# Kernel optimization log

Hardware: AMD Instinct MI355X
Metric: run time of the kernel (lower is better)

Reference implementation:

```python
import jax, jax.numpy as jnp
import numpy as np

B, T, D = 8, 2048, 1024
E, S = 8, 1            # num_experts, num_slots
FF = 4 * (S * D)       # ffn_mult * (num_slots * hiddens)

def setup_inputs() -> dict:
    key = jax.random.key(0)
    ks = jax.random.split(key, 7)
    sd = S * D
    inp = {
        "X":  jax.random.normal(ks[0], (B, T, D), dtype=jnp.float32),
        # slots gating MLP (single linear D -> E*S)
        "Wg": jax.random.normal(ks[1], (D, E * S), dtype=jnp.float32) / np.sqrt(D),
        "bg": jnp.zeros((E * S,), dtype=jnp.float32),
        # expert FFN (weights SHARED across experts, as in source [FFN(...)]*E)
        "W1": jax.random.normal(ks[2], (sd, FF), dtype=jnp.float32) / np.sqrt(sd),
        "b1": jnp.zeros((FF,), dtype=jnp.float32),
        "W2": jax.random.normal(ks[3], (FF, sd), dtype=jnp.float32) / np.sqrt(FF),
        "b2": jnp.zeros((sd,), dtype=jnp.float32),
    }
    return inp

def reference(X, Wg, bg, W1, b1, W2, b2):
    # logits: (B, T, E*S)
    logits = jnp.einsum('btd,de->bte', X, Wg) + bg
    dispatch_w = jax.nn.softmax(logits, axis=1)   # over tokens T
    combine_w = jax.nn.softmax(logits, axis=2)    # over slots E*S
    # slots = dispatch_w^T @ X : (B, E*S, D) -> (B, E, S*D)
    slots = jnp.einsum('bte,btd->bed', dispatch_w, X).reshape(B, E, S * D)
    # shared-weight FFN applied per expert slot (dropout=0 at eval)
    h = jax.nn.silu(jnp.einsum('bef,fh->beh', slots, W1) + b1)
    y = jnp.einsum('beh,hf->bef', h, W2) + b2     # (B, E, S*D)
    y = y.reshape(B, E * S, D)
    # combine: (B, T, E*S) @ (B, E*S, D)
    return jnp.einsum('bte,bed->btd', combine_w, y)
```

## Files before the change

kernel.cpp:

```cpp
#include <hip/hip_runtime.h>
#include <math.h>

#define B_  8
#define T_  2048
#define D_  1024
#define E_  8
#define FF_ 4096
#define N_  64
#define BT_ (B_*T_)

__global__ __launch_bounds__(256) void k_logits_part(
    const float* __restrict__ X, const float* __restrict__ Wg,
    float* __restrict__ part)
{
    __shared__ float xt[256 * 36];

    const int tid = threadIdx.x;
    const int bt0 = blockIdx.x * 256;
    const int d0  = blockIdx.y * 128;

    float acc[8];
    #pragma unroll
    for (int e = 0; e < 8; ++e) acc[e] = 0.f;

    for (int dt = 0; dt < 4; ++dt) {
        if (dt) __syncthreads();
        #pragma unroll
        for (int r = 0; r < 8; ++r) {
            int fi = r * 256 + tid;
            int token = fi >> 3, dj = fi & 7;
            const float4 v = *(const float4*)
                &X[(size_t)(bt0 + token) * D_ + d0 + dt * 32 + dj * 4];
            *(float4*)&xt[token * 36 + dj * 4] = v;
        }
        __syncthreads();
        #pragma unroll
        for (int dj = 0; dj < 8; ++dj) {
            const float4 x4 = *(const float4*)&xt[tid * 36 + dj * 4];
            const int db = d0 + dt * 32 + dj * 4;
            const float xv[4] = {x4.x, x4.y, x4.z, x4.w};
            #pragma unroll
            for (int r = 0; r < 4; ++r) {
                const float4 wlo = *(const float4*)&Wg[(size_t)(db + r) * 8];
                const float4 whi = *(const float4*)&Wg[(size_t)(db + r) * 8 + 4];
                acc[0] += xv[r] * wlo.x; acc[1] += xv[r] * wlo.y;
                acc[2] += xv[r] * wlo.z; acc[3] += xv[r] * wlo.w;
                acc[4] += xv[r] * whi.x; acc[5] += xv[r] * whi.y;
                acc[6] += xv[r] * whi.z; acc[7] += xv[r] * whi.w;
            }
        }
    }

    float* pp = &part[(size_t)blockIdx.y * BT_ * E_ + (size_t)(bt0 + tid) * E_];
    *(float4*)&pp[0] = make_float4(acc[0], acc[1], acc[2], acc[3]);
    *(float4*)&pp[4] = make_float4(acc[4], acc[5], acc[6], acc[7]);
}

__global__ __launch_bounds__(256) void k_logits_merge(
    const float* __restrict__ part, const float* __restrict__ bg,
    float* __restrict__ logits, float* __restrict__ sexp_part)
{
    __shared__ float red[8 * 256];
    const int tid = threadIdx.x;
    const int token = blockIdx.x * 256 + tid;

    float a[8];
    #pragma unroll
    for (int e = 0; e < 8; ++e) a[e] = 0.f;
    #pragma unroll
    for (int p = 0; p < 8; ++p) {
        const float* pp = &part[(size_t)p * BT_ * E_ + (size_t)token * E_];
        const float4 v0 = *(const float4*)&pp[0];
        const float4 v1 = *(const float4*)&pp[4];
        a[0] += v0.x; a[1] += v0.y; a[2] += v0.z; a[3] += v0.w;
        a[4] += v1.x; a[5] += v1.y; a[6] += v1.z; a[7] += v1.w;
    }
    #pragma unroll
    for (int e = 0; e < 8; ++e) a[e] += bg[e];

    float* lp = &logits[(size_t)token * E_];
    *(float4*)&lp[0] = make_float4(a[0], a[1], a[2], a[3]);
    *(float4*)&lp[4] = make_float4(a[4], a[5], a[6], a[7]);

    #pragma unroll
    for (int e = 0; e < 8; ++e) red[e * 256 + tid] = expf(a[e]);
    __syncthreads();
    for (int s = 128; s >= 1; s >>= 1) {
        if (tid < s) {
            #pragma unroll
            for (int e = 0; e < 8; ++e)
                red[e * 256 + tid] += red[e * 256 + tid + s];
        }
        __syncthreads();
    }
    if (tid < 8) sexp_part[blockIdx.x * 8 + tid] = red[tid * 256];
}

__global__ __launch_bounds__(256) void k_slots_part(
    const float* __restrict__ X, const float* __restrict__ logits,
    const float* __restrict__ sexp_part, float* __restrict__ part)
{
    __shared__ float wlds[64 * 8];
    __shared__ float red[64];
    __shared__ float inv[8];

    const int tid = threadIdx.x;
    const int ts = blockIdx.x, b = blockIdx.y;
    const int t0 = ts * 64;

    if (tid < 64) red[tid] = sexp_part[b * 64 + tid];
    __syncthreads();
    if (tid < 8) {
        float s = 0.f;
        #pragma unroll
        for (int i = 0; i < 8; ++i) s += red[i * 8 + tid];
        inv[tid] = 1.f / s;
    }
    __syncthreads();
    #pragma unroll
    for (int r = 0; r < 2; ++r) {
        int idx = r * 256 + tid;
        wlds[idx] = expf(logits[((size_t)b * T_ + t0) * E_ + idx]) * inv[idx & 7];
    }
    __syncthreads();

    float4 acc[8];
    #pragma unroll
    for (int e = 0; e < 8; ++e) { acc[e].x = acc[e].y = acc[e].z = acc[e].w = 0.f; }

    const float* xb = &X[((size_t)b * T_ + t0) * D_ + tid * 4];
    #pragma unroll 8
    for (int t = 0; t < 64; ++t) {
        const float4 x4 = *(const float4*)&xb[(size_t)t * D_];
        const float4 wA = *(const float4*)&wlds[t * 8];
        const float4 wB = *(const float4*)&wlds[t * 8 + 4];
        const float w[8] = {wA.x, wA.y, wA.z, wA.w, wB.x, wB.y, wB.z, wB.w};
        #pragma unroll
        for (int e = 0; e < 8; ++e) {
            acc[e].x += x4.x * w[e];
            acc[e].y += x4.y * w[e];
            acc[e].z += x4.z * w[e];
            acc[e].w += x4.w * w[e];
        }
    }
    #pragma unroll
    for (int e = 0; e < 8; ++e) {
        *(float4*)&part[(size_t)ts * (N_ * D_) + (size_t)(b * E_ + e) * D_ + tid * 4] = acc[e];
    }
}

__global__ __launch_bounds__(256) void k_reduce_slots(
    const float* __restrict__ part, float* __restrict__ slots)
{
    const int i = blockIdx.x * 256 + threadIdx.x;
    float s = 0.f;
    #pragma unroll
    for (int p = 0; p < 32; ++p) s += part[(size_t)p * (N_ * D_) + i];
    slots[i] = s;
}

__global__ __launch_bounds__(256) void k_gemm_part(
    const float* __restrict__ A, const float* __restrict__ W,
    float* __restrict__ part, int K, int F)
{
    __shared__ float As[64][128];

    const int tid = threadIdx.x;
    const int rg  = tid >> 5;
    const int cg  = tid & 31;
    const int f0  = blockIdx.x * 128 + cg * 4;
    const int k0  = blockIdx.y * 128;

    #pragma unroll
    for (int i = 0; i < 8; ++i) {
        int idx = i * 256 + tid;
        int row = idx >> 5, kq = idx & 31;
        const float4 v = *(const float4*)&A[(size_t)row * K + k0 + kq * 4];
        *(float4*)&As[row][kq * 4] = v;
    }
    __syncthreads();

    float4 acc[8];
    #pragma unroll
    for (int r = 0; r < 8; ++r) { acc[r].x = acc[r].y = acc[r].z = acc[r].w = 0.f; }

    #pragma unroll 2
    for (int kq = 0; kq < 32; ++kq) {
        float4 w0 = *(const float4*)&W[(size_t)(k0 + kq * 4 + 0) * F + f0];
        float4 w1 = *(const float4*)&W[(size_t)(k0 + kq * 4 + 1) * F + f0];
        float4 w2 = *(const float4*)&W[(size_t)(k0 + kq * 4 + 2) * F + f0];
        float4 w3 = *(const float4*)&W[(size_t)(k0 + kq * 4 + 3) * F + f0];
        #pragma unroll
        for (int r = 0; r < 8; ++r) {
            const float4 a = *(const float4*)&As[rg * 8 + r][kq * 4];
            acc[r].x += a.x * w0.x + a.y * w1.x + a.z * w2.x + a.w * w3.x;
            acc[r].y += a.x * w0.y + a.y * w1.y + a.z * w2.y + a.w * w3.y;
            acc[r].z += a.x * w0.z + a.y * w1.z + a.z * w2.z + a.w * w3.z;
            acc[r].w += a.x * w0.w + a.y * w1.w + a.z * w2.w + a.w * w3.w;
        }
    }

    float* pb = &part[(size_t)blockIdx.y * N_ * F];
    #pragma unroll
    for (int r = 0; r < 8; ++r)
        *(float4*)&pb[(size_t)(rg * 8 + r) * F + f0] = acc[r];
}

__global__ __launch_bounds__(256) void k_reduce_silu(
    const float* __restrict__ part, const float* __restrict__ b1,
    float* __restrict__ h)
{
    const int i = blockIdx.x * 256 + threadIdx.x;
    float s = 0.f;
    #pragma unroll
    for (int p = 0; p < 8; ++p) s += part[(size_t)p * (N_ * FF_) + i];
    s += b1[i & (FF_ - 1)];
    h[i] = s / (1.f + expf(-s));
}

__global__ __launch_bounds__(256) void k_reduce_bias(
    const float* __restrict__ part, const float* __restrict__ b2,
    float* __restrict__ y)
{
    const int i = blockIdx.x * 256 + threadIdx.x;
    float s = 0.f;
    #pragma unroll
    for (int p = 0; p < 32; ++p) s += part[(size_t)p * (N_ * D_) + i];
    y[i] = s + b2[i & (D_ - 1)];
}

__global__ __launch_bounds__(256) void k_combine(
    const float* __restrict__ logits, const float* __restrict__ y,
    float* __restrict__ out)
{
    __shared__ float wlds[64 * 8];
    const int tid = threadIdx.x;
    const int dc = blockIdx.x, tc = blockIdx.y, b = blockIdx.z;
    const int t0 = tc * 64;

    if (tid < 64) {
        const float* lp = &logits[((size_t)b * T_ + t0 + tid) * E_];
        float ex[8]; float s = 0.f;
        #pragma unroll
        for (int i = 0; i < 8; ++i) { ex[i] = expf(lp[i]); s += ex[i]; }
        const float invs = 1.f / s;
        #pragma unroll
        for (int i = 0; i < 8; ++i) wlds[tid * 8 + i] = ex[i] * invs;
    }
    __syncthreads();

    const int d = dc * 256 + tid;
    float yv[8];
    #pragma unroll
    for (int e = 0; e < 8; ++e) yv[e] = y[(size_t)(b * E_ + e) * D_ + d];

    for (int t = 0; t < 64; ++t) {
        const float4 wA = *(const float4*)&wlds[t * 8];
        const float4 wB = *(const float4*)&wlds[t * 8 + 4];
        const float acc = wA.x * yv[0] + wA.y * yv[1] + wA.z * yv[2] + wA.w * yv[3]
                        + wB.x * yv[4] + wB.y * yv[5] + wB.z * yv[6] + wB.w * yv[7];
        out[((size_t)b * T_ + t0 + t) * D_ + d] = acc;
    }
}

extern "C" void kernel_launch(void* const* d_in, const int* in_sizes, int n_in,
                              void* d_out, int out_size, void* d_ws, size_t ws_size,
                              hipStream_t stream)
{
    const float* X  = (const float*)d_in[0];
    const float* Wg = (const float*)d_in[1];
    const float* bg = (const float*)d_in[2];
    const float* W1 = (const float*)d_in[3];
    const float* b1 = (const float*)d_in[4];
    const float* W2 = (const float*)d_in[5];
    const float* b2 = (const float*)d_in[6];
    float* out = (float*)d_out;

    float* wsf       = (float*)d_ws;
    float* logits    = wsf;
    float* sexp_part = logits + BT_ * E_;
    float* slots     = sexp_part + 512;
    float* h         = slots + N_ * D_;
    float* y         = h + N_ * FF_;

    float* part = out;

    hipLaunchKernelGGL(k_logits_part,  dim3(BT_ / 256, 8), dim3(256), 0, stream,
                       X, Wg, part);
    hipLaunchKernelGGL(k_logits_merge, dim3(BT_ / 256),    dim3(256), 0, stream,
                       part, bg, logits, sexp_part);
    hipLaunchKernelGGL(k_slots_part,   dim3(32, 8),        dim3(256), 0, stream,
                       X, logits, sexp_part, part);
    hipLaunchKernelGGL(k_reduce_slots, dim3(256),          dim3(256), 0, stream,
                       part, slots);
    hipLaunchKernelGGL(k_gemm_part,    dim3(FF_ / 128, 1024 / 128), dim3(256), 0, stream,
                       slots, W1, part, 1024, FF_);
    hipLaunchKernelGGL(k_reduce_silu,  dim3(N_ * FF_ / 256), dim3(256), 0, stream,
                       part, b1, h);
    hipLaunchKernelGGL(k_gemm_part,    dim3(D_ / 128, FF_ / 128), dim3(256), 0, stream,
                       h, W2, part, FF_, D_);
    hipLaunchKernelGGL(k_reduce_bias,  dim3(N_ * D_ / 256), dim3(256), 0, stream,
                       part, b2, y);
    hipLaunchKernelGGL(k_combine,      dim3(4, 32, 8), dim3(256), 0, stream,
                       logits, y, out);
}
```

Before: 251.3 us.

## Replace split-K partial buffers with atomic accumulation and fuse bias into combine

After: 285.2 us. +13.5%, slower.

```diff
diff --git a/kernel.cpp b/kernel.cpp
--- a/kernel.cpp
+++ b/kernel.cpp
@@ -8,6 +8,11 @@
 #define FF_ 4096
 #define N_  64
 #define BT_ (B_*T_)
+
+#define LPART_F  0u
+#define HACC_F   0u
+#define H_F      262144u
+#define SPART_F  1048576u
 
 __global__ __launch_bounds__(256) void k_logits_part(
     const float* __restrict__ X, const float* __restrict__ Wg,
@@ -51,7 +56,8 @@
         }
     }
 
-    float* pp = &part[(size_t)blockIdx.y * BT_ * E_ + (size_t)(bt0 + tid) * E_];
+    float* pp = &part[LPART_F + (size_t)blockIdx.y * BT_ * E_
+                      + (size_t)(bt0 + tid) * E_];
     *(float4*)&pp[0] = make_float4(acc[0], acc[1], acc[2], acc[3]);
     *(float4*)&pp[4] = make_float4(acc[4], acc[5], acc[6], acc[7]);
 }
@@ -69,7 +75,8 @@
     for (int e = 0; e < 8; ++e) a[e] = 0.f;
     #pragma unroll
     for (int p = 0; p < 8; ++p) {
-        const float* pp = &part[(size_t)p * BT_ * E_ + (size_t)token * E_];
+        const float* pp = &part[LPART_F + (size_t)p * BT_ * E_
+                                + (size_t)token * E_];
         const float4 v0 = *(const float4*)&pp[0];
         const float4 v1 = *(const float4*)&pp[4];
         a[0] += v0.x; a[1] += v0.y; a[2] += v0.z; a[3] += v0.w;
@@ -100,13 +107,13 @@
     const float* __restrict__ X, const float* __restrict__ logits,
     const float* __restrict__ sexp_part, float* __restrict__ part)
 {
-    __shared__ float wlds[64 * 8];
+    __shared__ float wlds[32 * 8];
     __shared__ float red[64];
     __shared__ float inv[8];
 
     const int tid = threadIdx.x;
     const int ts = blockIdx.x, b = blockIdx.y;
-    const int t0 = ts * 64;
+    const int t0 = ts * 32;
 
     if (tid < 64) red[tid] = sexp_part[b * 64 + tid];
     __syncthreads();
@@ -117,20 +124,19 @@
         inv[tid] = 1.f / s;
     }
     __syncthreads();
-    #pragma unroll
-    for (int r = 0; r < 2; ++r) {
-        int idx = r * 256 + tid;
-        wlds[idx] = expf(logits[((size_t)b * T_ + t0) * E_ + idx]) * inv[idx & 7];
+    {
+        int t = tid >> 3, e = tid & 7;
+        wlds[tid] = expf(logits[((size_t)b * T_ + t0 + t) * E_ + e]) * inv[e];
     }
     __syncthreads();
 
     float4 acc[8];
     #pragma unroll
-    for (int e = 0; e < 8; ++e) { acc[e].x = acc[e].y = acc[e].z = acc[e].w = 0.f; }
+    for (int e = 0; e < 8; ++e) acc[e] = make_float4(0.f, 0.f, 0.f, 0.f);
 
     const float* xb = &X[((size_t)b * T_ + t0) * D_ + tid * 4];
     #pragma unroll 8
-    for (int t = 0; t < 64; ++t) {
+    for (int t = 0; t < 32; ++t) {
         const float4 x4 = *(const float4*)&xb[(size_t)t * D_];
         const float4 wA = *(const float4*)&wlds[t * 8];
         const float4 wB = *(const float4*)&wlds[t * 8 + 4];
@@ -145,7 +151,8 @@
     }
     #pragma unroll
     for (int e = 0; e < 8; ++e) {
-        *(float4*)&part[(size_t)ts * (N_ * D_) + (size_t)(b * E_ + e) * D_ + tid * 4] = acc[e];
+        *(float4*)&part[SPART_F + (size_t)ts * (N_ * D_)
+                        + (size_t)(b * E_ + e) * D_ + tid * 4] = acc[e];
     }
 }
 
@@ -155,83 +162,82 @@
     const int i = blockIdx.x * 256 + threadIdx.x;
     float s = 0.f;
     #pragma unroll
-    for (int p = 0; p < 32; ++p) s += part[(size_t)p * (N_ * D_) + i];
+    for (int p = 0; p < 64; ++p)
+        s += part[SPART_F + (size_t)p * (N_ * D_) + i];
     slots[i] = s;
 }
 
-__global__ __launch_bounds__(256) void k_gemm_part(
+template<int K, int F>
+__global__ __launch_bounds__(256) void k_gemm_atomic(
     const float* __restrict__ A, const float* __restrict__ W,
-    float* __restrict__ part, int K, int F)
-{
-    __shared__ float As[64][128];
-
-    const int tid = threadIdx.x;
-    const int rg  = tid >> 5;
-    const int cg  = tid & 31;
-    const int f0  = blockIdx.x * 128 + cg * 4;
-    const int k0  = blockIdx.y * 128;
+    float* __restrict__ outp)
+{
+    __shared__ float As[64 * 132];
+
+    const int tid = threadIdx.x;
+    const int rg = tid >> 4, cg = tid & 15;
+    const int f0 = blockIdx.x * 64 + cg * 4;
+    const int k0 = blockIdx.y * 128;
 
     #pragma unroll
     for (int i = 0; i < 8; ++i) {
         int idx = i * 256 + tid;
         int row = idx >> 5, kq = idx & 31;
-        const float4 v = *(const float4*)&A[(size_t)row * K + k0 + kq * 4];
-        *(float4*)&As[row][kq * 4] = v;
-    }
-    __syncthreads();
-
-    float4 acc[8];
-    #pragma unroll
-    for (int r = 0; r < 8; ++r) { acc[r].x = acc[r].y = acc[r].z = acc[r].w = 0.f; }
+        *(float4*)&As[row * 132 + kq * 4] =
+            *(const float4*)&A[(size_t)row * K + k0 + kq * 4];
+    }
+    __syncthreads();
+
+    float4 acc[4];
+    #pragma unroll
+    for (int r = 0; r < 4; ++r) acc[r] = make_float4(0.f, 0.f, 0.f, 0.f);
 
     #pragma unroll 2
     for (int kq = 0; kq < 32; ++kq) {
-        float4 w0 = *(const float4*)&W[(size_t)(k0 + kq * 4 + 0) * F + f0];
-        float4 w1 = *(const float4*)&W[(size_t)(k0 + kq * 4 + 1) * F + f0];
-        float4 w2 = *(const float4*)&W[(size_t)(k0 + kq * 4 + 2) * F + f0];
-        float4 w3 = *(const float4*)&W[(size_t)(k0 + kq * 4 + 3) * F + f0];
-        #pragma unroll
-        for (int r = 0; r < 8; ++r) {
-            const float4 a = *(const float4*)&As[rg * 8 + r][kq * 4];
-            acc[r].x += a.x * w0.x + a.y * w1.x + a.z * w2.x + a.w * w3.x;
-            acc[r].y += a.x * w0.y + a.y * w1.y + a.z * w2.y + a.w * w3.y;
-            acc[r].z += a.x * w0.z + a.y * w1.z + a.z * w2.z + a.w * w3.z;
-            acc[r].w += a.x * w0.w + a.y * w1.w + a.z * w2.w + a.w * w3.w;
-        }
-    }
-
-    float* pb = &part[(size_t)blockIdx.y * N_ * F];
-    #pragma unroll
-    for (int r = 0; r < 8; ++r)
-        *(float4*)&pb[(size_t)(rg * 8 + r) * F + f0] = acc[r];
-}
-
-__global__ __launch_bounds__(256) void k_reduce_silu(
-    const float* __restrict__ part, const float* __restrict__ b1,
+        const float* wr = &W[(size_t)(k0 + kq * 4) * F + f0];
+        const float4 w0 = *(const float4*)&wr[0];
+        const float4 w1 = *(const float4*)&wr[(size_t)F];
+        const float4 w2 = *(const float4*)&wr[2 * (size_t)F];
+        const float4 w3 = *(const float4*)&wr[3 * (size_t)F];
+        #pragma unroll
+        for (int r = 0; r < 4; ++r) {
+            const float4 a = *(const float4*)&As[(rg * 4 + r) * 132 + kq * 4];
+            acc[r].x += a.x*w0.x + a.y*w1.x + a.z*w2.x + a.w*w3.x;
+            acc[r].y += a.x*w0.y + a.y*w1.y + a.z*w2.y + a.w*w3.y;
+            acc[r].z += a.x*w0.z + a.y*w1.z + a.z*w2.z + a.w*w3.z;
+            acc[r].w += a.x*w0.w + a.y*w1.w + a.z*w2.w + a.w*w3.w;
+        }
+    }
+
+    #pragma unroll
+    for (int r = 0; r < 4; ++r) {
+        float* op = &outp[(size_t)(rg * 4 + r) * F + f0];
+        unsafeAtomicAdd(&op[0], acc[r].x);
+        unsafeAtomicAdd(&op[1], acc[r].y);
+        unsafeAtomicAdd(&op[2], acc[r].z);
+        unsafeAtomicAdd(&op[3], acc[r].w);
+    }
+}
+
+__global__ __launch_bounds__(256) void k_silu(
+    const float* __restrict__ hacc, const float* __restrict__ b1,
     float* __restrict__ h)
 {
-    const int i = blockIdx.x * 256 + threadIdx.x;
-    float s = 0.f;
-    #pragma unroll
-    for (int p = 0; p < 8; ++p) s += part[(size_t)p * (N_ * FF_) + i];
-    s += b1[i & (FF_ - 1)];
-    h[i] = s / (1.f + expf(-s));
-}
-
-__global__ __launch_bounds__(256) void k_reduce_bias(
-    const float* __restrict__ part, const float* __restrict__ b2,
-    float* __restrict__ y)
-{
-    const int i = blockIdx.x * 256 + threadIdx.x;
-    float s = 0.f;
-    #pragma unroll
-    for (int p = 0; p < 32; ++p) s += part[(size_t)p * (N_ * D_) + i];
-    y[i] = s + b2[i & (D_ - 1)];
+    const int i4 = blockIdx.x * 256 + threadIdx.x;
+    const float4 v = *(const float4*)&hacc[(size_t)i4 * 4];
+    const float4 bb = *(const float4*)&b1[(i4 * 4) & (FF_ - 1)];
+    float4 r;
+    r.x = v.x + bb.x; r.y = v.y + bb.y; r.z = v.z + bb.z; r.w = v.w + bb.w;
+    r.x = r.x / (1.f + expf(-r.x));
+    r.y = r.y / (1.f + expf(-r.y));
+    r.z = r.z / (1.f + expf(-r.z));
+    r.w = r.w / (1.f + expf(-r.w));
+    *(float4*)&h[(size_t)i4 * 4] = r;
 }
 
 __global__ __launch_bounds__(256) void k_combine(
-    const float* __restrict__ logits, const float* __restrict__ y,
-    float* __restrict__ out)
+    const float* __restrict__ logits, const float* __restrict__ yacc,
+    const float* __restrict__ b2, float* __restrict__ out)
 {
     __shared__ float wlds[64 * 8];
     const int tid = threadIdx.x;
@@ -250,15 +256,17 @@
     __syncthreads();
 
     const int d = dc * 256 + tid;
+    const float bv = b2[d];
     float yv[8];
     #pragma unroll
-    for (int e = 0; e < 8; ++e) yv[e] = y[(size_t)(b * E_ + e) * D_ + d];
+    for (int e = 0; e < 8; ++e)
+        yv[e] = yacc[(size_t)(b * E_ + e) * D_ + d] + bv;
 
     for (int t = 0; t < 64; ++t) {
         const float4 wA = *(const float4*)&wlds[t * 8];
         const float4 wB = *(const float4*)&wlds[t * 8 + 4];
-        const float acc = wA.x * yv[0] + wA.y * yv[1] + wA.z * yv[2] + wA.w * yv[3]
-                        + wB.x * yv[4] + wB.y * yv[5] + wB.z * yv[6] + wB.w * yv[7];
+        const float acc = wA.x*yv[0] + wA.y*yv[1] + wA.z*yv[2] + wA.w*yv[3]
+                        + wB.x*yv[4] + wB.y*yv[5] + wB.z*yv[6] + wB.w*yv[7];
         out[((size_t)b * T_ + t0 + t) * D_ + d] = acc;
     }
 }
@@ -280,27 +288,27 @@
     float* logits    = wsf;
     float* sexp_part = logits + BT_ * E_;
     float* slots     = sexp_part + 512;
-    float* h         = slots + N_ * D_;
-    float* y         = h + N_ * FF_;
-
-    float* part = out;
+    float* yacc      = slots + N_ * D_;
+
+    float* hacc = out + HACC_F;
+    float* h    = out + H_F;
 
     hipLaunchKernelGGL(k_logits_part,  dim3(BT_ / 256, 8), dim3(256), 0, stream,
-                       X, Wg, part);
+                       X, Wg, out);
     hipLaunchKernelGGL(k_logits_merge, dim3(BT_ / 256),    dim3(256), 0, stream,
-                       part, bg, logits, sexp_part);
-    hipLaunchKernelGGL(k_slots_part,   dim3(32, 8),        dim3(256), 0, stream,
-                       X, logits, sexp_part, part);
+                       out, bg, logits, sexp_part);
+    hipLaunchKernelGGL(k_slots_part,   dim3(64, 8),        dim3(256), 0, stream,
+                       X, logits, sexp_part, out);
     hipLaunchKernelGGL(k_reduce_slots, dim3(256),          dim3(256), 0, stream,
-                       part, slots);
-    hipLaunchKernelGGL(k_gemm_part,    dim3(FF_ / 128, 1024 / 128), dim3(256), 0, stream,
-                       slots, W1, part, 1024, FF_);
-    hipLaunchKernelGGL(k_reduce_silu,  dim3(N_ * FF_ / 256), dim3(256), 0, stream,
-                       part, b1, h);
-    hipLaunchKernelGGL(k_gemm_part,    dim3(D_ / 128, FF_ / 128), dim3(256), 0, stream,
-                       h, W2, part, FF_, D_);
-    hipLaunchKernelGGL(k_reduce_bias,  dim3(N_ * D_ / 256), dim3(256), 0, stream,
-                       part, b2, y);
+                       out, slots);
+    hipMemsetAsync(hacc, 0, (size_t)N_ * FF_ * sizeof(float), stream);
+    hipMemsetAsync(yacc, 0, (size_t)N_ * D_ * sizeof(float), stream);
+    hipLaunchKernelGGL((k_gemm_atomic<1024, 4096>), dim3(FF_ / 64, 1024 / 128),
+                       dim3(256), 0, stream, slots, W1, hacc);
+    hipLaunchKernelGGL(k_silu,         dim3(N_ * FF_ / 1024), dim3(256), 0, stream,
+                       hacc, b1, h);
+    hipLaunchKernelGGL((k_gemm_atomic<4096, 1024>), dim3(D_ / 64, FF_ / 128),
+                       dim3(256), 0, stream, h, W2, yacc);
     hipLaunchKernelGGL(k_combine,      dim3(4, 32, 8), dim3(256), 0, stream,
-                       logits, y, out);
-}
+                       logits, yacc, b2, out);
+}
```
